# Kernel optimization log

Measured on AMD Instinct MI355X. Metric: run time of the kernel, lower is better.

Reference implementation:

```python
import jax, jax.numpy as jnp
import numpy as np

GRID_SIZE = 8
MARGIN = 1.0
NUM_NEG = 8
SOS_NEG = 8
LOSS_LAMBDA = 1.0
D_INTER = 4  # d1_inter_num == d2_inter_num == 4 in the source
IMG = 512    # image side in pixels (H * grid_size)


def warp_points(pts, homo):
    ph = jnp.concatenate([pts, jnp.ones_like(pts[..., :1])], axis=-1)  # B,N,3
    q = jnp.einsum('bij,bnj->bni', homo, ph)
    return q[..., :2] / (q[..., 2:3] + 1e-8)


def inv_sim_vec(d1, d2):
    # 2 - 2*<d1,d2> == squared L2 distance for unit-norm descriptors
    return 2.0 - 2.0 * jnp.sum(d1 * d2, axis=-1)


def inv_sim_mat(d1, d2):
    return 2.0 - 2.0 * jnp.einsum('bnc,bmc->bnm', d1, d2)


def sq_dist_mat(p1, p2):
    # squared Euclidean distance; monotone in distance so topk indices and
    # radius comparisons (vs radius**2) match the original exactly.
    n1 = jnp.sum(p1 * p1, axis=-1)
    n2 = jnp.sum(p2 * p2, axis=-1)
    d = n1[:, :, None] + n2[:, None, :] - 2.0 * jnp.einsum('bnd,bmd->bnm', p1, p2)
    return jnp.maximum(d, 0.0)


def topk_smallest(x, k):
    v, i = jax.lax.top_k(-x, k)
    return -v, i


def create_coo_grid(h, w, grid_size):
    ys, xs = jnp.meshgrid(jnp.arange(h, dtype=jnp.float32), jnp.arange(w, dtype=jnp.float32), indexing='ij')
    return jnp.stack([(xs + 0.5) * grid_size, (ys + 0.5) * grid_size], axis=-1).reshape(-1, 2)  # HW,2 (x,y)


def sample_descriptors(desc, kp, grid_size):
    # desc: B,C,H,W; kp: B,N,2 (x,y) image coords. Bilinear sample + L2 normalize.
    b, c, h, w = desc.shape
    x = kp[..., 0] / grid_size - 0.5
    y = kp[..., 1] / grid_size - 0.5
    x0 = jnp.floor(x); y0 = jnp.floor(y)
    wx = x - x0; wy = y - y0
    x0i = jnp.clip(x0.astype(jnp.int32), 0, w - 1); x1i = jnp.clip(x0i + 1, 0, w - 1)
    y0i = jnp.clip(y0.astype(jnp.int32), 0, h - 1); y1i = jnp.clip(y0i + 1, 0, h - 1)
    dflat = desc.transpose(0, 2, 3, 1).reshape(b, h * w, c)  # B,HW,C
    bi = jnp.arange(b)[:, None]
    g = lambda yi, xi: dflat[bi, yi * w + xi]  # B,N,C
    out = ((1 - wx) * (1 - wy))[..., None] * g(y0i, x0i) \
        + (wx * (1 - wy))[..., None] * g(y0i, x1i) \
        + ((1 - wx) * wy)[..., None] * g(y1i, x0i) \
        + (wx * wy)[..., None] * g(y1i, x1i)
    return out / (jnp.linalg.norm(out, axis=-1, keepdims=True) + 1e-8)


def setup_inputs():
    key = jax.random.key(0)
    k1, k2, k3, k4 = jax.random.split(key, 4)
    b, n, c, h, w = 4, 1024, 128, 64, 64
    kp1 = jax.random.uniform(k1, (b, n, 2), dtype=jnp.float32) * (IMG - 1.0)
    kp1_desc = jax.random.normal(k2, (b, n, c), dtype=jnp.float32)
    kp1_desc = kp1_desc / jnp.linalg.norm(kp1_desc, axis=-1, keepdims=True)
    desc2 = jax.random.normal(k3, (b, c, h, w), dtype=jnp.float32)
    homo12 = jnp.broadcast_to(jnp.eye(3, dtype=jnp.float32), (b, 3, 3)) + 0.005 * jax.random.normal(k4, (b, 3, 3), dtype=jnp.float32)
    w_kp1 = jnp.clip(warp_points(kp1, homo12), 0.0, IMG - 1.0)
    return {'kp1': kp1, 'w_kp1': w_kp1, 'kp1_desc': kp1_desc, 'desc2': desc2, 'homo12': homo12}


def reference(kp1, w_kp1, kp1_desc, desc2, homo12):
    b, n, c = kp1_desc.shape
    _, _, h, w = desc2.shape
    hw = h * w
    gs = GRID_SIZE
    bi = jnp.arange(b)[:, None]

    w_kp1_desc = sample_descriptors(desc2, w_kp1, gs)                 # B,N,C
    positive_sim = inv_sim_vec(kp1_desc, w_kp1_desc)                  # B,N

    coo = jnp.broadcast_to(create_coo_grid(h, w, gs), (b, hw, 2))     # B,HW,2
    # 4 nearest grid cells of each kp1, warped into image 2
    _, kp1_cell_ids = topk_smallest(sq_dist_mat(kp1, coo), D_INTER)   # B,N,4
    kp1_cells = coo[bi, kp1_cell_ids.reshape(b, -1)]                  # B,4N,2
    w_kp1_cells = warp_points(kp1_cells, homo12)                      # B,4N,2
    _, kp2_cell_ids = topk_smallest(sq_dist_mat(w_kp1_cells, coo), D_INTER)  # B,4N,4
    mask = jnp.zeros((b, n * D_INTER, hw), dtype=jnp.float32)
    mask = mask.at[jnp.arange(b)[:, None, None], jnp.arange(n * D_INTER)[None, :, None], kp2_cell_ids].set(1.0)
    neigh_mask = mask.reshape(b, n, D_INTER, hw).sum(axis=2)          # B,N,HW

    desc2_flat = desc2.transpose(0, 2, 3, 1).reshape(b, hw, c)
    desc_sim = inv_sim_mat(kp1_desc, desc2_flat) + neigh_mask * 5.0   # B,N,HW
    neg_sim, _ = topk_smallest(desc_sim, NUM_NEG)                     # B,N,num_neg
    fos = jnp.mean(jnp.maximum(positive_sim[:, :, None] - neg_sim + MARGIN, 0.0) ** 2)

    radius2 = (gs * np.sqrt(2.0) + 0.1) ** 2
    kp1_sim = inv_sim_mat(kp1_desc, kp1_desc) + (sq_dist_mat(kp1, kp1) <= radius2).astype(jnp.float32) * 5.0
    w_kp1_sim = inv_sim_mat(w_kp1_desc, w_kp1_desc) + (sq_dist_mat(w_kp1, w_kp1) <= radius2).astype(jnp.float32) * 5.0
    _, kp1_neg_ids = topk_smallest(kp1_sim, SOS_NEG)                  # B,N,sos_neg
    _, w_kp1_neg_ids = topk_smallest(w_kp1_sim, SOS_NEG)
    b3 = jnp.arange(b)[:, None, None]
    kp1_neg_desc = kp1_desc[b3, kp1_neg_ids]                          # B,N,sos_neg,C
    w_kp1_neg_desc = w_kp1_desc[b3, w_kp1_neg_ids]
    sos = inv_sim_vec(kp1_desc[:, :, None, :], kp1_neg_desc) - inv_sim_vec(w_kp1_desc[:, :, None, :], w_kp1_neg_desc)
    sos = jnp.mean(jnp.sqrt(jnp.sum(sos ** 2, axis=-1)))
    return (fos + sos) * LOSS_LAMBDA
```

## Files before the change

### kernel.cpp

```cpp
#include <hip/hip_runtime.h>

#define NB 4
#define NN 1024
#define NCCH 128
#define NH 64
#define NW 64
#define NHW 4096
#define CHUNK 128

constexpr float RADIUS2 = 130.27274173013714f;

typedef __attribute__((ext_vector_type(8))) short short8v;
typedef __attribute__((ext_vector_type(4))) float f32x4;

__device__ __forceinline__ unsigned short f2bf(float f) {
    unsigned u = __float_as_uint(f);
    unsigned r = u + 0x7FFFu + ((u >> 16) & 1u);
    return (unsigned short)(r >> 16);
}
__device__ __forceinline__ float bf2f(unsigned short h) {
    return __uint_as_float(((unsigned)h) << 16);
}

__device__ __forceinline__ void bsort8(float* v) {
    #pragma unroll
    for (int d = 4; d >= 1; d >>= 1) {
        #pragma unroll
        for (int i = 0; i < 8; ++i) {
            if ((i & d) == 0) {
                float x = v[i], y = v[i + d];
                v[i] = fminf(x, y);
                v[i + d] = fmaxf(x, y);
            }
        }
    }
}
__device__ __forceinline__ void merge8(const float* a, const float* b, float* o) {
    #pragma unroll
    for (int k = 0; k < 8; ++k) o[k] = fminf(a[k], b[7 - k]);
    bsort8(o);
}

__device__ __forceinline__ void nearest4(float x, float y, int out_ids[4]) {
    float u = x * 0.125f - 0.5f;
    float v = y * 0.125f - 0.5f;
    u = fminf(fmaxf(u, -1e6f), 1e6f);
    v = fminf(fmaxf(v, -1e6f), 1e6f);
    int iu = (int)floorf(u);
    int iv = (int)floorf(v);
    int xlo = min(max(iu - 2, 0), 60);
    int xhi = max(min(iu + 3, 63), 3);
    int ylo = min(max(iv - 2, 0), 60);
    int yhi = max(min(iv + 3, 63), 3);
    float bd0 = 1e30f, bd1 = 1e30f, bd2 = 1e30f, bd3 = 1e30f;
    int bi0 = 0, bi1 = 0, bi2 = 0, bi3 = 0;
    for (int yy = ylo; yy <= yhi; ++yy) {
        float dy = y - ((float)yy + 0.5f) * 8.0f;
        float dy2 = dy * dy;
        for (int xx = xlo; xx <= xhi; ++xx) {
            float dx = x - ((float)xx + 0.5f) * 8.0f;
            float d = dx * dx + dy2;
            int id = (yy << 6) | xx;
            if (d < bd3) {
                if (d < bd2) {
                    bd3 = bd2; bi3 = bi2;
                    if (d < bd1) {
                        bd2 = bd1; bi2 = bi1;
                        if (d < bd0) { bd1 = bd0; bi1 = bi0; bd0 = d; bi0 = id; }
                        else         { bd1 = d;  bi1 = id; }
                    } else { bd2 = d; bi2 = id; }
                } else { bd3 = d; bi3 = id; }
            }
        }
    }
    out_ids[0] = bi0; out_ids[1] = bi1; out_ids[2] = bi2; out_ids[3] = bi3;
}

__global__ __launch_bounds__(256) void d2split_kernel(
    const float* __restrict__ desc2,
    unsigned short* __restrict__ d2hi, unsigned short* __restrict__ d2lo,
    float* __restrict__ d2T, int use_t)
{
    __shared__ float sT[64][33];
    int bid = blockIdx.x;
    int b = bid >> 8;
    int rem = bid & 255;
    int hw0 = (rem >> 2) * 64;
    int c0 = (rem & 3) * 32;
    int t = threadIdx.x;

    {
        int lane = t & 63, cg = t >> 6;
        const float* src = desc2 + (size_t)b * NCCH * NHW + hw0 + lane;
        #pragma unroll
        for (int i = 0; i < 8; ++i) {
            int cl = cg * 8 + i;
            sT[lane][cl] = src[(size_t)(c0 + cl) * NHW];
        }
    }
    __syncthreads();
    {
        int hw = t >> 2, q = t & 3;
        size_t base = ((size_t)b * NHW + hw0 + hw) * NCCH + c0 + q * 8;
        unsigned short hb[8], lb[8];
        float fb[8];
        #pragma unroll
        for (int i = 0; i < 8; ++i) {
            float f = sT[hw][q * 8 + i];
            unsigned short h = f2bf(f);
            hb[i] = h;
            lb[i] = f2bf(f - bf2f(h));
            fb[i] = f;
        }
        *(short8v*)(d2hi + base) = *(short8v*)hb;
        *(short8v*)(d2lo + base) = *(short8v*)lb;
        if (use_t) {
            *(float4*)(d2T + base) = *(float4*)&fb[0];
            *(float4*)(d2T + base + 4) = *(float4*)&fb[4];
        }
    }
}

__global__ __launch_bounds__(256) void sample_mask_kernel(
    const float* __restrict__ kp1, const float* __restrict__ w_kp1,
    const float* __restrict__ kp1_desc, const float* __restrict__ desc2,
    const float* __restrict__ d2T, int use_t,
    const float* __restrict__ homo,
    unsigned short* __restrict__ khi, unsigned short* __restrict__ klo,
    unsigned short* __restrict__ whi, unsigned short* __restrict__ wlo,
    float* __restrict__ pos_sim, int* __restrict__ mask_ids)
{
    int bid = blockIdx.x;
    if (bid >= 1024) {
        int g = (bid - 1024) * 256 + threadIdx.x;
        if (g >= NB * NN) return;
        int b = g >> 10;
        float x = kp1[g * 2], y = kp1[g * 2 + 1];
        const float* H = homo + b * 9;
        int c4[4];
        nearest4(x, y, c4);
        int out[16];
        #pragma unroll
        for (int k = 0; k < 4; ++k) {
            int id = c4[k];
            float cx = ((float)(id & 63) + 0.5f) * 8.0f;
            float cy = ((float)(id >> 6) + 0.5f) * 8.0f;
            float q0 = H[0] * cx + H[1] * cy + H[2];
            float q1 = H[3] * cx + H[4] * cy + H[5];
            float q2 = H[6] * cx + H[7] * cy + H[8];
            float iz = 1.0f / (q2 + 1e-8f);
            nearest4(q0 * iz, q1 * iz, out + 4 * k);
        }
        #pragma unroll
        for (int k = 0; k < 16; ++k) mask_ids[(size_t)g * 16 + k] = out[k];
        return;
    }

    int lane = threadIdx.x & 63;
    int wid = bid * 4 + (threadIdx.x >> 6);
    int b = wid >> 10;

    float px = w_kp1[wid * 2 + 0], py = w_kp1[wid * 2 + 1];
    float fx = px * 0.125f - 0.5f, fy = py * 0.125f - 0.5f;
    float fx0 = floorf(fx), fy0 = floorf(fy);
    float wx = fx - fx0, wy = fy - fy0;
    int x0 = min(max((int)fx0, 0), NW - 1);
    int x1 = min(x0 + 1, NW - 1);
    int y0 = min(max((int)fy0, 0), NH - 1);
    int y1 = min(y0 + 1, NH - 1);
    float w00 = (1.f - wx) * (1.f - wy), w01 = wx * (1.f - wy);
    float w10 = (1.f - wx) * wy,         w11 = wx * wy;
    int i00 = y0 * NW + x0, i01 = y0 * NW + x1;
    int i10 = y1 * NW + x0, i11 = y1 * NW + x1;

    float o0, o1;
    if (use_t) {
        const float* base = d2T + (size_t)b * NHW * NCCH;
        const float* r00 = base + (size_t)i00 * NCCH;
        const float* r01 = base + (size_t)i01 * NCCH;
        const float* r10 = base + (size_t)i10 * NCCH;
        const float* r11 = base + (size_t)i11 * NCCH;
        o0 = w00 * r00[lane] + w01 * r01[lane] + w10 * r10[lane] + w11 * r11[lane];
        o1 = w00 * r00[lane + 64] + w01 * r01[lane + 64]
           + w10 * r10[lane + 64] + w11 * r11[lane + 64];
    } else {
        const float* d2 = desc2 + (size_t)b * NCCH * NHW;
        const float* p0 = d2 + (size_t)lane * NHW;
        const float* p1 = d2 + (size_t)(lane + 64) * NHW;
        o0 = w00 * p0[i00] + w01 * p0[i01] + w10 * p0[i10] + w11 * p0[i11];
        o1 = w00 * p1[i00] + w01 * p1[i01] + w10 * p1[i10] + w11 * p1[i11];
    }
    float nrm = o0 * o0 + o1 * o1;
    #pragma unroll
    for (int off = 32; off > 0; off >>= 1) nrm += __shfl_xor(nrm, off, 64);
    float inv = 1.0f / (sqrtf(nrm) + 1e-8f);
    o0 *= inv; o1 *= inv;

    float a0 = kp1_desc[(size_t)wid * NCCH + lane];
    float a1 = kp1_desc[(size_t)wid * NCCH + lane + 64];
    float dot = a0 * o0 + a1 * o1;
    #pragma unroll
    for (int off = 32; off > 0; off >>= 1) dot += __shfl_xor(dot, off, 64);

    size_t base = (size_t)wid * NCCH;
    unsigned short h;
    h = f2bf(a0); khi[base + lane] = h;      klo[base + lane] = f2bf(a0 - bf2f(h));
    h = f2bf(a1); khi[base + lane + 64] = h; klo[base + lane + 64] = f2bf(a1 - bf2f(h));
    h = f2bf(o0); whi[base + lane] = h;      wlo[base + lane] = f2bf(o0 - bf2f(h));
    h = f2bf(o1); whi[base + lane + 64] = h; wlo[base + lane + 64] = f2bf(o1 - bf2f(h));
    if (lane == 0) pos_sim[wid] = 2.0f - 2.0f * dot;
}

__global__ __launch_bounds__(256, 4) void simtop_fused(
    const unsigned short* __restrict__ khi, const unsigned short* __restrict__ klo,
    const unsigned short* __restrict__ whi, const unsigned short* __restrict__ wlo,
    const unsigned short* __restrict__ d2hi, const unsigned short* __restrict__ d2lo,
    const float* __restrict__ kp1, const float* __restrict__ w_kp1,
    const int* __restrict__ mask_ids,
    float* __restrict__ fosP, float* __restrict__ sosAP, float* __restrict__ sosBP)
{
    __shared__ float sChunk[32][CHUNK + 1];
    __shared__ int   sMask[32][16];
    __shared__ float sCx[CHUNK], sCy[CHUNK];
    __shared__ float sRx[32], sRy[32];

    int tid = threadIdx.x;
    int bid = blockIdx.x;
    int xcd = bid & 7, slot = bid >> 3;
    int gl = slot >> 5, rg = slot & 31;

    int mode, cs, b, nchunk, colbase, outStride;
    const unsigned short *AH, *AL, *BH, *BL;
    const float* coords = nullptr;
    float* outP;
    if (gl < 2) {
        int g = xcd + 8 * gl;
        mode = 0; b = g >> 2; cs = g & 3;
        nchunk = 8; colbase = cs * 1024;
        AH = khi + (size_t)b * NN * NCCH;  AL = klo + (size_t)b * NN * NCCH;
        BH = d2hi + (size_t)b * NHW * NCCH; BL = d2lo + (size_t)b * NHW * NCCH;
        outP = fosP; outStride = 32;
    } else if (gl == 2) {
        mode = 1; b = xcd >> 1; cs = xcd & 1;
        nchunk = 4; colbase = cs * 512;
        AH = khi + (size_t)b * NN * NCCH;  AL = klo + (size_t)b * NN * NCCH;
        BH = AH; BL = AL;
        coords = kp1; outP = sosAP; outStride = 16;
    } else {
        mode = 2; b = xcd >> 1; cs = xcd & 1;
        nchunk = 4; colbase = cs * 512;
        AH = whi + (size_t)b * NN * NCCH;  AL = wlo + (size_t)b * NN * NCCH;
        BH = AH; BL = AL;
        coords = w_kp1; outP = sosBP; outStride = 16;
    }
    int row0 = rg * 32;

    int lane = tid & 63, wg = tid >> 6;
    int lrow = lane & 15, lgrp = lane >> 4;
    int srow = tid & 31, sgrp = tid >> 5;

    short8v ahi[2][4], alo[2][4];
    #pragma unroll
    for (int rt = 0; rt < 2; ++rt) {
        const unsigned short* aH = AH + (size_t)(row0 + rt * 16 + lrow) * NCCH + lgrp * 8;
        const unsigned short* aL = AL + (size_t)(row0 + rt * 16 + lrow) * NCCH + lgrp * 8;
        #pragma unroll
        for (int s = 0; s < 4; ++s) {
            ahi[rt][s] = *(const short8v*)(aH + s * 32);
            alo[rt][s] = *(const short8v*)(aL + s * 32);
        }
    }

    if (mode == 0) {
        for (int e = tid; e < 512; e += 256)
            sMask[e >> 4][e & 15] =
                mask_ids[((size_t)b * NN + row0 + (e >> 4)) * 16 + (e & 15)];
    } else if (tid < 32) {
        sRx[tid] = coords[((size_t)b * NN + row0 + tid) * 2];
        sRy[tid] = coords[((size_t)b * NN + row0 + tid) * 2 + 1];
    }

    float loc[8];
    #pragma unroll
    for (int k = 0; k < 8; ++k) loc[k] = 1e30f;

    for (int ch = 0; ch < nchunk; ++ch) {
        int cglob = colbase + ch * CHUNK;
        __syncthreads();

        int colq = cglob + wg * 32;
        {
            const unsigned short* b0H = BH + (size_t)(colq + lrow) * NCCH + lgrp * 8;
            const unsigned short* b0L = BL + (size_t)(colq + lrow) * NCCH + lgrp * 8;
            const unsigned short* b1H = BH + (size_t)(colq + 16 + lrow) * NCCH + lgrp * 8;
            const unsigned short* b1L = BL + (size_t)(colq + 16 + lrow) * NCCH + lgrp * 8;
            f32x4 a00 = {0.f, 0.f, 0.f, 0.f}, a01 = {0.f, 0.f, 0.f, 0.f};
            f32x4 a10 = {0.f, 0.f, 0.f, 0.f}, a11 = {0.f, 0.f, 0.f, 0.f};
            #pragma unroll
            for (int s = 0; s < 4; ++s) {
                short8v bh0 = *(const short8v*)(b0H + s * 32);
                short8v bl0 = *(const short8v*)(b0L + s * 32);
                short8v bh1 = *(const short8v*)(b1H + s * 32);
                short8v bl1 = *(const short8v*)(b1L + s * 32);
                a00 = __builtin_amdgcn_mfma_f32_16x16x32_bf16(ahi[0][s], bh0, a00, 0, 0, 0);
                a10 = __builtin_amdgcn_mfma_f32_16x16x32_bf16(ahi[1][s], bh0, a10, 0, 0, 0);
                a01 = __builtin_amdgcn_mfma_f32_16x16x32_bf16(ahi[0][s], bh1, a01, 0, 0, 0);
                a11 = __builtin_amdgcn_mfma_f32_16x16x32_bf16(ahi[1][s], bh1, a11, 0, 0, 0);
                a00 = __builtin_amdgcn_mfma_f32_16x16x32_bf16(ahi[0][s], bl0, a00, 0, 0, 0);
                a10 = __builtin_amdgcn_mfma_f32_16x16x32_bf16(ahi[1][s], bl0, a10, 0, 0, 0);
                a01 = __builtin_amdgcn_mfma_f32_16x16x32_bf16(ahi[0][s], bl1, a01, 0, 0, 0);
                a11 = __builtin_amdgcn_mfma_f32_16x16x32_bf16(ahi[1][s], bl1, a11, 0, 0, 0);
                a00 = __builtin_amdgcn_mfma_f32_16x16x32_bf16(alo[0][s], bh0, a00, 0, 0, 0);
                a10 = __builtin_amdgcn_mfma_f32_16x16x32_bf16(alo[1][s], bh0, a10, 0, 0, 0);
                a01 = __builtin_amdgcn_mfma_f32_16x16x32_bf16(alo[0][s], bh1, a01, 0, 0, 0);
                a11 = __builtin_amdgcn_mfma_f32_16x16x32_bf16(alo[1][s], bh1, a11, 0, 0, 0);
            }
            #pragma unroll
            for (int r = 0; r < 4; ++r) {
                sChunk[lgrp * 4 + r][wg * 32 + lrow]           = 2.0f - 2.0f * a00[r];
                sChunk[16 + lgrp * 4 + r][wg * 32 + lrow]      = 2.0f - 2.0f * a10[r];
                sChunk[lgrp * 4 + r][wg * 32 + 16 + lrow]      = 2.0f - 2.0f * a01[r];
                sChunk[16 + lgrp * 4 + r][wg * 32 + 16 + lrow] = 2.0f - 2.0f * a11[r];
            }
        }
        __syncthreads();

        if (mode == 0) {
            for (int e = tid; e < 512; e += 256) {
                int r = e >> 4;
                int id = sMask[r][e & 15] - cglob;
                if (id >= 0 && id < CHUNK) atomicAdd(&sChunk[r][id], 5.0f);
            }
        } else {
            if (tid < CHUNK)
                sCx[tid] = coords[((size_t)b * NN + cglob + tid) * 2];
            else
                sCy[tid - CHUNK] = coords[((size_t)b * NN + cglob + (tid - CHUNK)) * 2 + 1];
        }
        __syncthreads();

        float rx = 0.f, ry = 0.f;
        if (mode != 0) { rx = sRx[srow]; ry = sRy[srow]; }
        #pragma unroll
        for (int j = 0; j < 16; ++j) {
            int cl = sgrp * 16 + j;
            float v = sChunk[srow][cl];
            if (mode != 0) {
                float dx = rx - sCx[cl], dy = ry - sCy[cl];
                if (dx * dx + dy * dy <= RADIUS2) v += 5.0f;
            }
            if (v < loc[7]) {
                loc[7] = v;
                #pragma unroll
                for (int p = 7; p > 0; --p) {
                    if (loc[p - 1] > loc[p]) {
                        float t = loc[p - 1]; loc[p - 1] = loc[p]; loc[p] = t;
                    }
                }
            }
        }
    }

    __syncthreads();
    float* mg = &sChunk[0][0];
    #pragma unroll
    for (int k = 0; k < 8; ++k) mg[srow * 67 + sgrp * 8 + k] = loc[k];
    __syncthreads();
    #pragma unroll
    for (int step = 1; step < 8; step <<= 1) {
        if ((sgrp & (2 * step - 1)) == 0) {
            float a[8], bb[8], o[8];
            #pragma unroll
            for (int k = 0; k < 8; ++k) {
                a[k]  = mg[srow * 67 + sgrp * 8 + k];
                bb[k] = mg[srow * 67 + (sgrp + step) * 8 + k];
            }
            merge8(a, bb, o);
            #pragma unroll
            for (int k = 0; k < 8; ++k) mg[srow * 67 + sgrp * 8 + k] = o[k];
        }
        __syncthreads();
    }
    if (tid < 32) {
        size_t row = (size_t)b * NN + row0 + tid;
        #pragma unroll
        for (int k = 0; k < 8; ++k)
            outP[row * outStride + cs * 8 + k] = mg[tid * 67 + k];
    }
}

__global__ __launch_bounds__(256) void frow_kernel(
    const float* __restrict__ fosP, const float* __restrict__ sosAP,
    const float* __restrict__ sosBP, const float* __restrict__ pos_sim,
    float* __restrict__ frow, float* __restrict__ srow)
{
    int row = blockIdx.x * 256 + threadIdx.x;
    if (row >= NB * NN) return;

    float l0[8], l1[8], l2[8], l3[8], t0[8], t1[8], m[8];
    const float4* fp = (const float4*)(fosP + (size_t)row * 32);
    float4 q;
    q = fp[0]; l0[0]=q.x; l0[1]=q.y; l0[2]=q.z; l0[3]=q.w;
    q = fp[1]; l0[4]=q.x; l0[5]=q.y; l0[6]=q.z; l0[7]=q.w;
    q = fp[2]; l1[0]=q.x; l1[1]=q.y; l1[2]=q.z; l1[3]=q.w;
    q = fp[3]; l1[4]=q.x; l1[5]=q.y; l1[6]=q.z; l1[7]=q.w;
    q = fp[4]; l2[0]=q.x; l2[1]=q.y; l2[2]=q.z; l2[3]=q.w;
    q = fp[5]; l2[4]=q.x; l2[5]=q.y; l2[6]=q.z; l2[7]=q.w;
    q = fp[6]; l3[0]=q.x; l3[1]=q.y; l3[2]=q.z; l3[3]=q.w;
    q = fp[7]; l3[4]=q.x; l3[5]=q.y; l3[6]=q.z; l3[7]=q.w;
    merge8(l0, l1, t0); merge8(l2, l3, t1); merge8(t0, t1, m);

    float p = pos_sim[row], fs = 0.f;
    #pragma unroll
    for (int k = 0; k < 8; ++k) {
        float h = fmaxf(p - m[k] + 1.0f, 0.f);
        fs += h * h;
    }

    const float4* ap = (const float4*)(sosAP + (size_t)row * 16);
    q = ap[0]; l0[0]=q.x; l0[1]=q.y; l0[2]=q.z; l0[3]=q.w;
    q = ap[1]; l0[4]=q.x; l0[5]=q.y; l0[6]=q.z; l0[7]=q.w;
    q = ap[2]; l1[0]=q.x; l1[1]=q.y; l1[2]=q.z; l1[3]=q.w;
    q = ap[3]; l1[4]=q.x; l1[5]=q.y; l1[6]=q.z; l1[7]=q.w;
    merge8(l0, l1, t0);
    const float4* bp = (const float4*)(sosBP + (size_t)row * 16);
    q = bp[0]; l2[0]=q.x; l2[1]=q.y; l2[2]=q.z; l2[3]=q.w;
    q = bp[1]; l2[4]=q.x; l2[5]=q.y; l2[6]=q.z; l2[7]=q.w;
    q = bp[2]; l3[0]=q.x; l3[1]=q.y; l3[2]=q.z; l3[3]=q.w;
    q = bp[3]; l3[4]=q.x; l3[5]=q.y; l3[6]=q.z; l3[7]=q.w;
    merge8(l2, l3, t1);

    float acc = 0.f;
    #pragma unroll
    for (int k = 0; k < 8; ++k) {
        float d = t0[k] - t1[k];
        acc += d * d;
    }
    frow[row] = fs;
    srow[row] = sqrtf(acc);
}

__global__ __launch_bounds__(256) void freduce_kernel(
    const float* __restrict__ frow, const float* __restrict__ srow,
    float* __restrict__ outp)
{
    __shared__ float sf[256], ss[256];
    int t = threadIdx.x;
    float f = 0.f, s = 0.f;
    for (int i = t; i < NB * NN; i += 256) { f += frow[i]; s += srow[i]; }
    sf[t] = f; ss[t] = s;
    __syncthreads();
    for (int o = 128; o > 0; o >>= 1) {
        if (t < o) { sf[t] += sf[t + o]; ss[t] += ss[t + o]; }
        __syncthreads();
    }
    if (t == 0)
        outp[0] = sf[0] / (float)(NB * NN * 8) + ss[0] / (float)(NB * NN);
}

extern "C" void kernel_launch(void* const* d_in, const int* in_sizes, int n_in,
                              void* d_out, int out_size, void* d_ws, size_t ws_size,
                              hipStream_t stream) {
    const float* kp1      = (const float*)d_in[0];
    const float* w_kp1    = (const float*)d_in[1];
    const float* kp1_desc = (const float*)d_in[2];
    const float* desc2    = (const float*)d_in[3];
    const float* homo     = (const float*)d_in[4];
    float* outp = (float*)d_out;

    char* ws = (char*)d_ws;
    size_t o = 0;
    unsigned short* khi  = (unsigned short*)(ws + o); o += (size_t)NB * NN * NCCH * 2;
    unsigned short* klo  = (unsigned short*)(ws + o); o += (size_t)NB * NN * NCCH * 2;
    unsigned short* whi  = (unsigned short*)(ws + o); o += (size_t)NB * NN * NCCH * 2;
    unsigned short* wlo  = (unsigned short*)(ws + o); o += (size_t)NB * NN * NCCH * 2;
    unsigned short* d2hi = (unsigned short*)(ws + o); o += (size_t)NB * NHW * NCCH * 2;
    unsigned short* d2lo = (unsigned short*)(ws + o); o += (size_t)NB * NHW * NCCH * 2;
    float* pos_sim = (float*)(ws + o); o += (size_t)NB * NN * 4;
    float* fosP    = (float*)(ws + o); o += (size_t)NB * NN * 32 * 4;
    float* sosAP   = (float*)(ws + o); o += (size_t)NB * NN * 16 * 4;
    float* sosBP   = (float*)(ws + o); o += (size_t)NB * NN * 16 * 4;
    float* frow    = (float*)(ws + o); o += (size_t)NB * NN * 4;
    float* srow    = (float*)(ws + o); o += (size_t)NB * NN * 4;
    int*   mask_id = (int*)(ws + o);   o += (size_t)NB * NN * 16 * 4;
    float* d2T     = (float*)(ws + o);
    size_t need_t  = o + (size_t)NB * NHW * NCCH * 4;
    int use_t = (ws_size >= need_t) ? 1 : 0;
    if (!use_t) d2T = (float*)ws;

    d2split_kernel<<<NB * 256, 256, 0, stream>>>(desc2, d2hi, d2lo, d2T, use_t);
    sample_mask_kernel<<<1040, 256, 0, stream>>>(kp1, w_kp1, kp1_desc, desc2,
                                                 d2T, use_t, homo,
                                                 khi, klo, whi, wlo,
                                                 pos_sim, mask_id);
    simtop_fused<<<1024, 256, 0, stream>>>(khi, klo, whi, wlo, d2hi, d2lo,
                                           kp1, w_kp1, mask_id,
                                           fosP, sosAP, sosBP);
    frow_kernel<<<16, 256, 0, stream>>>(fosP, sosAP, sosBP, pos_sim, frow, srow);
    freduce_kernel<<<1, 256, 0, stream>>>(frow, srow, outp);
}
```

Before: 177.2 us.

## Merge prep kernels, drop transposed fp32 copy, split fos columns finer

```diff
diff --git a/kernel.cpp b/kernel.cpp
--- a/kernel.cpp
+++ b/kernel.cpp
@@ -76,63 +76,53 @@
     out_ids[0] = bi0; out_ids[1] = bi1; out_ids[2] = bi2; out_ids[3] = bi3;
 }
 
-__global__ __launch_bounds__(256) void d2split_kernel(
-    const float* __restrict__ desc2,
+__global__ __launch_bounds__(256) void prep_kernel(
+    const float* __restrict__ kp1, const float* __restrict__ w_kp1,
+    const float* __restrict__ kp1_desc, const float* __restrict__ desc2,
+    const float* __restrict__ homo,
+    unsigned short* __restrict__ khi, unsigned short* __restrict__ klo,
+    unsigned short* __restrict__ whi, unsigned short* __restrict__ wlo,
     unsigned short* __restrict__ d2hi, unsigned short* __restrict__ d2lo,
-    float* __restrict__ d2T, int use_t)
+    float* __restrict__ pos_sim, int* __restrict__ mask_ids)
 {
     __shared__ float sT[64][33];
     int bid = blockIdx.x;
-    int b = bid >> 8;
-    int rem = bid & 255;
-    int hw0 = (rem >> 2) * 64;
-    int c0 = (rem & 3) * 32;
     int t = threadIdx.x;
 
-    {
-        int lane = t & 63, cg = t >> 6;
-        const float* src = desc2 + (size_t)b * NCCH * NHW + hw0 + lane;
-        #pragma unroll
-        for (int i = 0; i < 8; ++i) {
-            int cl = cg * 8 + i;
-            sT[lane][cl] = src[(size_t)(c0 + cl) * NHW];
-        }
-    }
-    __syncthreads();
-    {
-        int hw = t >> 2, q = t & 3;
-        size_t base = ((size_t)b * NHW + hw0 + hw) * NCCH + c0 + q * 8;
-        unsigned short hb[8], lb[8];
-        float fb[8];
-        #pragma unroll
-        for (int i = 0; i < 8; ++i) {
-            float f = sT[hw][q * 8 + i];
-            unsigned short h = f2bf(f);
-            hb[i] = h;
-            lb[i] = f2bf(f - bf2f(h));
-            fb[i] = f;
-        }
-        *(short8v*)(d2hi + base) = *(short8v*)hb;
-        *(short8v*)(d2lo + base) = *(short8v*)lb;
-        if (use_t) {
-            *(float4*)(d2T + base) = *(float4*)&fb[0];
-            *(float4*)(d2T + base + 4) = *(float4*)&fb[4];
-        }
-    }
-}
-
-__global__ __launch_bounds__(256) void sample_mask_kernel(
-    const float* __restrict__ kp1, const float* __restrict__ w_kp1,
-    const float* __restrict__ kp1_desc, const float* __restrict__ desc2,
-    const float* __restrict__ d2T, int use_t,
-    const float* __restrict__ homo,
-    unsigned short* __restrict__ khi, unsigned short* __restrict__ klo,
-    unsigned short* __restrict__ whi, unsigned short* __restrict__ wlo,
-    float* __restrict__ pos_sim, int* __restrict__ mask_ids)
-{
-    int bid = blockIdx.x;
-    if (bid >= 1024) {
-        int g = (bid - 1024) * 256 + threadIdx.x;
+    if (bid < 1024) {
+        int b = bid >> 8;
+        int rem = bid & 255;
+        int hw0 = (rem >> 2) * 64;
+        int c0 = (rem & 3) * 32;
+        {
+            int lane = t & 63, cg = t >> 6;
+            const float* src = desc2 + (size_t)b * NCCH * NHW + hw0 + lane;
+            #pragma unroll
+            for (int i = 0; i < 8; ++i) {
+                int cl = cg * 8 + i;
+                sT[lane][cl] = src[(size_t)(c0 + cl) * NHW];
+            }
+        }
+        __syncthreads();
+        {
+            int hw = t >> 2, q = t & 3;
+            size_t base = ((size_t)b * NHW + hw0 + hw) * NCCH + c0 + q * 8;
+            unsigned short hb[8], lb[8];
+            #pragma unroll
+            for (int i = 0; i < 8; ++i) {
+                float f = sT[hw][q * 8 + i];
+                unsigned short h = f2bf(f);
+                hb[i] = h;
+                lb[i] = f2bf(f - bf2f(h));
+            }
+            *(short8v*)(d2hi + base) = *(short8v*)hb;
+            *(short8v*)(d2lo + base) = *(short8v*)lb;
+        }
+        return;
+    }
+
+    if (bid >= 2048) {
+        int g = (bid - 2048) * 256 + t;
         if (g >= NB * NN) return;
         int b = g >> 10;
         float x = kp1[g * 2], y = kp1[g * 2 + 1];
@@ -156,8 +146,8 @@
         return;
     }
 
-    int lane = threadIdx.x & 63;
-    int wid = bid * 4 + (threadIdx.x >> 6);
+    int lane = t & 63;
+    int wid = (bid - 1024) * 4 + (t >> 6);
     int b = wid >> 10;
 
     float px = w_kp1[wid * 2 + 0], py = w_kp1[wid * 2 + 1];
@@ -173,23 +163,11 @@
     int i00 = y0 * NW + x0, i01 = y0 * NW + x1;
     int i10 = y1 * NW + x0, i11 = y1 * NW + x1;
 
-    float o0, o1;
-    if (use_t) {
-        const float* base = d2T + (size_t)b * NHW * NCCH;
-        const float* r00 = base + (size_t)i00 * NCCH;
-        const float* r01 = base + (size_t)i01 * NCCH;
-        const float* r10 = base + (size_t)i10 * NCCH;
-        const float* r11 = base + (size_t)i11 * NCCH;
-        o0 = w00 * r00[lane] + w01 * r01[lane] + w10 * r10[lane] + w11 * r11[lane];
-        o1 = w00 * r00[lane + 64] + w01 * r01[lane + 64]
-           + w10 * r10[lane + 64] + w11 * r11[lane + 64];
-    } else {
-        const float* d2 = desc2 + (size_t)b * NCCH * NHW;
-        const float* p0 = d2 + (size_t)lane * NHW;
-        const float* p1 = d2 + (size_t)(lane + 64) * NHW;
-        o0 = w00 * p0[i00] + w01 * p0[i01] + w10 * p0[i10] + w11 * p0[i11];
-        o1 = w00 * p1[i00] + w01 * p1[i01] + w10 * p1[i10] + w11 * p1[i11];
-    }
+    const float* d2 = desc2 + (size_t)b * NCCH * NHW;
+    const float* p0 = d2 + (size_t)lane * NHW;
+    const float* p1 = d2 + (size_t)(lane + 64) * NHW;
+    float o0 = w00 * p0[i00] + w01 * p0[i01] + w10 * p0[i10] + w11 * p0[i11];
+    float o1 = w00 * p1[i00] + w01 * p1[i01] + w10 * p1[i10] + w11 * p1[i11];
     float nrm = o0 * o0 + o1 * o1;
     #pragma unroll
     for (int off = 32; off > 0; off >>= 1) nrm += __shfl_xor(nrm, off, 64);
@@ -229,26 +207,26 @@
     int xcd = bid & 7, slot = bid >> 3;
     int gl = slot >> 5, rg = slot & 31;
 
-    int mode, cs, b, nchunk, colbase, outStride;
+    int mode, cs, b, colbase, outStride;
     const unsigned short *AH, *AL, *BH, *BL;
     const float* coords = nullptr;
     float* outP;
-    if (gl < 2) {
+    if (gl < 4) {
         int g = xcd + 8 * gl;
-        mode = 0; b = g >> 2; cs = g & 3;
-        nchunk = 8; colbase = cs * 1024;
+        mode = 0; b = g >> 3; cs = g & 7;
+        colbase = cs * 512;
         AH = khi + (size_t)b * NN * NCCH;  AL = klo + (size_t)b * NN * NCCH;
         BH = d2hi + (size_t)b * NHW * NCCH; BL = d2lo + (size_t)b * NHW * NCCH;
-        outP = fosP; outStride = 32;
-    } else if (gl == 2) {
+        outP = fosP; outStride = 64;
+    } else if (gl == 4) {
         mode = 1; b = xcd >> 1; cs = xcd & 1;
-        nchunk = 4; colbase = cs * 512;
+        colbase = cs * 512;
         AH = khi + (size_t)b * NN * NCCH;  AL = klo + (size_t)b * NN * NCCH;
         BH = AH; BL = AL;
         coords = kp1; outP = sosAP; outStride = 16;
     } else {
         mode = 2; b = xcd >> 1; cs = xcd & 1;
-        nchunk = 4; colbase = cs * 512;
+        colbase = cs * 512;
         AH = whi + (size_t)b * NN * NCCH;  AL = wlo + (size_t)b * NN * NCCH;
         BH = AH; BL = AL;
         coords = w_kp1; outP = sosBP; outStride = 16;
@@ -284,7 +262,7 @@
     #pragma unroll
     for (int k = 0; k < 8; ++k) loc[k] = 1e30f;
 
-    for (int ch = 0; ch < nchunk; ++ch) {
+    for (int ch = 0; ch < 4; ++ch) {
         int cglob = colbase + ch * CHUNK;
         __syncthreads();
 
@@ -397,18 +375,21 @@
     int row = blockIdx.x * 256 + threadIdx.x;
     if (row >= NB * NN) return;
 
-    float l0[8], l1[8], l2[8], l3[8], t0[8], t1[8], m[8];
-    const float4* fp = (const float4*)(fosP + (size_t)row * 32);
-    float4 q;
-    q = fp[0]; l0[0]=q.x; l0[1]=q.y; l0[2]=q.z; l0[3]=q.w;
-    q = fp[1]; l0[4]=q.x; l0[5]=q.y; l0[6]=q.z; l0[7]=q.w;
-    q = fp[2]; l1[0]=q.x; l1[1]=q.y; l1[2]=q.z; l1[3]=q.w;
-    q = fp[3]; l1[4]=q.x; l1[5]=q.y; l1[6]=q.z; l1[7]=q.w;
-    q = fp[4]; l2[0]=q.x; l2[1]=q.y; l2[2]=q.z; l2[3]=q.w;
-    q = fp[5]; l2[4]=q.x; l2[5]=q.y; l2[6]=q.z; l2[7]=q.w;
-    q = fp[6]; l3[0]=q.x; l3[1]=q.y; l3[2]=q.z; l3[3]=q.w;
-    q = fp[7]; l3[4]=q.x; l3[5]=q.y; l3[6]=q.z; l3[7]=q.w;
-    merge8(l0, l1, t0); merge8(l2, l3, t1); merge8(t0, t1, m);
+    float La[8][8];
+    {
+        const float4* fp = (const float4*)(fosP + (size_t)row * 64);
+        #pragma unroll
+        for (int li = 0; li < 8; ++li) {
+            float4 qa = fp[2 * li], qb = fp[2 * li + 1];
+            La[li][0] = qa.x; La[li][1] = qa.y; La[li][2] = qa.z; La[li][3] = qa.w;
+            La[li][4] = qb.x; La[li][5] = qb.y; La[li][6] = qb.z; La[li][7] = qb.w;
+        }
+    }
+    float t0[8], t1[8], t2[8], t3[8], u0[8], u1[8], m[8];
+    merge8(La[0], La[1], t0); merge8(La[2], La[3], t1);
+    merge8(La[4], La[5], t2); merge8(La[6], La[7], t3);
+    merge8(t0, t1, u0); merge8(t2, t3, u1);
+    merge8(u0, u1, m);
 
     float p = pos_sim[row], fs = 0.f;
     #pragma unroll
@@ -417,6 +398,8 @@
         fs += h * h;
     }
 
+    float l0[8], l1[8];
+    float4 q;
     const float4* ap = (const float4*)(sosAP + (size_t)row * 16);
     q = ap[0]; l0[0]=q.x; l0[1]=q.y; l0[2]=q.z; l0[3]=q.w;
     q = ap[1]; l0[4]=q.x; l0[5]=q.y; l0[6]=q.z; l0[7]=q.w;
@@ -424,11 +407,11 @@
     q = ap[3]; l1[4]=q.x; l1[5]=q.y; l1[6]=q.z; l1[7]=q.w;
     merge8(l0, l1, t0);
     const float4* bp = (const float4*)(sosBP + (size_t)row * 16);
-    q = bp[0]; l2[0]=q.x; l2[1]=q.y; l2[2]=q.z; l2[3]=q.w;
-    q = bp[1]; l2[4]=q.x; l2[5]=q.y; l2[6]=q.z; l2[7]=q.w;
-    q = bp[2]; l3[0]=q.x; l3[1]=q.y; l3[2]=q.z; l3[3]=q.w;
-    q = bp[3]; l3[4]=q.x; l3[5]=q.y; l3[6]=q.z; l3[7]=q.w;
-    merge8(l2, l3, t1);
+    q = bp[0]; l0[0]=q.x; l0[1]=q.y; l0[2]=q.z; l0[3]=q.w;
+    q = bp[1]; l0[4]=q.x; l0[5]=q.y; l0[6]=q.z; l0[7]=q.w;
+    q = bp[2]; l1[0]=q.x; l1[1]=q.y; l1[2]=q.z; l1[3]=q.w;
+    q = bp[3]; l1[4]=q.x; l1[5]=q.y; l1[6]=q.z; l1[7]=q.w;
+    merge8(l0, l1, t1);
 
     float acc = 0.f;
     #pragma unroll
@@ -477,23 +460,17 @@
     unsigned short* d2hi = (unsigned short*)(ws + o); o += (size_t)NB * NHW * NCCH * 2;
     unsigned short* d2lo = (unsigned short*)(ws + o); o += (size_t)NB * NHW * NCCH * 2;
     float* pos_sim = (float*)(ws + o); o += (size_t)NB * NN * 4;
-    float* fosP    = (float*)(ws + o); o += (size_t)NB * NN * 32 * 4;
+    float* fosP    = (float*)(ws + o); o += (size_t)NB * NN * 64 * 4;
     float* sosAP   = (float*)(ws + o); o += (size_t)NB * NN * 16 * 4;
     float* sosBP   = (float*)(ws + o); o += (size_t)NB * NN * 16 * 4;
     float* frow    = (float*)(ws + o); o += (size_t)NB * NN * 4;
     float* srow    = (float*)(ws + o); o += (size_t)NB * NN * 4;
     int*   mask_id = (int*)(ws + o);   o += (size_t)NB * NN * 16 * 4;
-    float* d2T     = (float*)(ws + o);
-    size_t need_t  = o + (size_t)NB * NHW * NCCH * 4;
-    int use_t = (ws_size >= need_t) ? 1 : 0;
-    if (!use_t) d2T = (float*)ws;
-
-    d2split_kernel<<<NB * 256, 256, 0, stream>>>(desc2, d2hi, d2lo, d2T, use_t);
-    sample_mask_kernel<<<1040, 256, 0, stream>>>(kp1, w_kp1, kp1_desc, desc2,
-                                                 d2T, use_t, homo,
-                                                 khi, klo, whi, wlo,
-                                                 pos_sim, mask_id);
-    simtop_fused<<<1024, 256, 0, stream>>>(khi, klo, whi, wlo, d2hi, d2lo,
+
+    prep_kernel<<<2064, 256, 0, stream>>>(kp1, w_kp1, kp1_desc, desc2, homo,
+                                          khi, klo, whi, wlo, d2hi, d2lo,
+                                          pos_sim, mask_id);
+    simtop_fused<<<1536, 256, 0, stream>>>(khi, klo, whi, wlo, d2hi, d2lo,
                                            kp1, w_kp1, mask_id,
                                            fosP, sosAP, sosBP);
     frow_kernel<<<16, 256, 0, stream>>>(fosP, sosAP, sosBP, pos_sim, frow, srow);
```

Result: no change. 174.7 us (-1.4%).
